# Performance work log

Hardware: AMD Instinct MI355X
Metric: run time of the kernel (lower is better)

## Reference

```python
import jax, jax.numpy as jnp
import numpy as np

DIM, E_DIM, HID = 512, 1024, 256
N_EXP, N_MIC, TOP_K, TOP_K_MIC = 8, 325, 2, 8
EPS_LN = 1e-5


def _layernorm(x, g, b):
    mu = x.mean(-1, keepdims=True)
    var = ((x - mu) ** 2).mean(-1, keepdims=True)
    return (x - mu) / jnp.sqrt(var + EPS_LN) * g + b


def setup_inputs() -> dict:
    key = jax.random.key(0)
    ks = jax.random.split(key, 20)
    s = 0.02
    return {
        "x": jax.random.normal(ks[0], (2, 512, DIM), jnp.float32),
        "router_w": jax.random.normal(ks[1], (N_EXP, DIM), jnp.float32) * s,
        "router_b": jnp.zeros((N_EXP,), jnp.float32),
        "exp_w1": jax.random.normal(ks[2], (N_EXP, E_DIM, DIM), jnp.float32) * s,
        "exp_b1": jnp.zeros((N_EXP, E_DIM), jnp.float32),
        "exp_w2": jax.random.normal(ks[3], (N_EXP, DIM, E_DIM), jnp.float32) * s,
        "exp_b2": jnp.zeros((N_EXP, DIM), jnp.float32),
        "mrouter_w": jax.random.normal(ks[4], (N_MIC, DIM), jnp.float32) * s,
        "mrouter_b": jnp.zeros((N_MIC,), jnp.float32),
        "mic_w1": jax.random.normal(ks[5], (N_MIC, HID, DIM), jnp.float32) * s,
        "mic_b1": jnp.zeros((N_MIC, HID), jnp.float32),
        "mic_w2": jax.random.normal(ks[6], (N_MIC, DIM, HID), jnp.float32) * s,
        "mic_b2": jnp.zeros((N_MIC, DIM), jnp.float32),
        "mic_g": jnp.ones((N_MIC, DIM), jnp.float32),
        "mic_beta": jnp.zeros((N_MIC, DIM), jnp.float32),
        "norm_g": jnp.ones((DIM,), jnp.float32),
        "norm_b": jnp.zeros((DIM,), jnp.float32),
    }


def _forward(x, router_w, router_b, exp_w1, exp_b1, exp_w2, exp_b2,
             mrouter_w, mrouter_b, mic_w1, mic_b1, mic_w2, mic_b2,
             mic_g, mic_beta, norm_g, norm_b):
    B, S, D = x.shape
    xf = x.reshape(-1, D)  # [T, D]

    # ---- expert routing (top-2 of 8) ----
    probs = jax.nn.softmax(xf @ router_w.T + router_b, axis=-1)
    topp, topi = jax.lax.top_k(probs, TOP_K)
    topp = topp / (topp.sum(-1, keepdims=True) + 1e-8)

    # dense compute over 8 experts, combine with top-k weights
    h = jax.nn.gelu(jnp.einsum('td,ehd->teh', xf, exp_w1) + exp_b1, approximate=False)
    ye = jnp.einsum('teh,edh->ted', h, exp_w2) + exp_b2  # [T, E, D]
    comb_w = (jax.nn.one_hot(topi, N_EXP, dtype=xf.dtype) * topp[..., None]).sum(1)  # [T, E]
    eo = jnp.einsum('te,ted->td', comb_w, ye)

    # ---- micro routing (top-8 of 325) ----
    mprobs = jax.nn.softmax(eo @ mrouter_w.T + mrouter_b, axis=-1)
    mtopp, mtopi = jax.lax.top_k(mprobs, TOP_K_MIC)
    mtopp = mtopp / (mtopp.sum(-1, keepdims=True) + 1e-8)

    def micro_slot(eo, p, idx):
        # gather per-token micro params, batched GEMV dispatch
        hm = jax.nn.gelu(jnp.einsum('td,thd->th', eo, mic_w1[idx]) + mic_b1[idx],
                         approximate=False)
        ym = jnp.einsum('th,tdh->td', hm, mic_w2[idx]) + mic_b2[idx]
        n = _layernorm(eo + ym, mic_g[idx], mic_beta[idx])
        return p[:, None] * n

    micro_slot = jax.checkpoint(micro_slot, static_argnums=())
    mo = jnp.zeros_like(eo)
    for k in range(TOP_K_MIC):  # small fixed loop over slots
        mo = mo + micro_slot(eo, mtopp[:, k], mtopi[:, k])

    combined = (eo + 0.1 * mo).reshape(B, S, D)
    return _layernorm(combined, norm_g, norm_b)


def reference(x, router_w, router_b, exp_w1, exp_b1, exp_w2, exp_b2,
              mrouter_w, mrouter_b, mic_w1, mic_b1, mic_w2, mic_b2,
              mic_g, mic_beta, norm_g, norm_b):
    return _forward(x, router_w, router_b, exp_w1, exp_b1, exp_w2, exp_b2,
                    mrouter_w, mrouter_b, mic_w1, mic_b1, mic_w2, mic_b2,
                    mic_g, mic_beta, norm_g, norm_b)
```

## Files before the change

kernel.cpp:

```cpp
#include <hip/hip_runtime.h>
#include <hip/hip_bf16.h>
#include <math.h>

#define T_TOK 1024
#define DIMM  512
#define EDIM  1024
#define HIDD  256
#define NEXP  8
#define NMIC  325
#define E16TILES 136
#define MTILES  840
#define NPAIR_M 8192

typedef __attribute__((ext_vector_type(8))) short bf16x8;
typedef __attribute__((ext_vector_type(4))) float f32x4;

__device__ __forceinline__ float dot4(float4 a, float4 b) {
    return a.x*b.x + a.y*b.y + a.z*b.z + a.w*b.w;
}
__device__ __forceinline__ float gelu_exact(float x) {
    return 0.5f * x * (1.0f + erff(x * 0.70710678118654752f));
}
__device__ __forceinline__ float wave_sum(float v) {
    #pragma unroll
    for (int o = 32; o; o >>= 1) v += __shfl_xor(v, o);
    return v;
}
__device__ __forceinline__ short f2bf(float f) {
    union { __hip_bfloat16 h; short s; } u;
    u.h = __float2bfloat16(f);
    return u.s;
}
__device__ __forceinline__ bf16x8 cvt8(float4 a, float4 b) {
    bf16x8 r;
    r[0]=f2bf(a.x); r[1]=f2bf(a.y); r[2]=f2bf(a.z); r[3]=f2bf(a.w);
    r[4]=f2bf(b.x); r[5]=f2bf(b.y); r[6]=f2bf(b.z); r[7]=f2bf(b.w);
    return r;
}

__global__ void k_router(const float* __restrict__ x, const float* __restrict__ rw,
                         const float* __restrict__ rb, int* __restrict__ eidx,
                         float* __restrict__ ew, int* __restrict__ ecnt) {
    int wave = threadIdx.x >> 6, lane = threadIdx.x & 63;
    int t = blockIdx.x * 4 + wave;
    if (t >= T_TOK) return;
    const float* xr = x + (size_t)t * DIMM;
    float xv[8];
    #pragma unroll
    for (int j = 0; j < 8; ++j) xv[j] = xr[lane + 64*j];
    float p[NEXP];
    #pragma unroll
    for (int e = 0; e < NEXP; ++e) {
        const float* wr = rw + (size_t)e * DIMM;
        float a = 0.f;
        #pragma unroll
        for (int j = 0; j < 8; ++j) a += xv[j] * wr[lane + 64*j];
        p[e] = wave_sum(a) + rb[e];
    }
    float m = p[0];
    #pragma unroll
    for (int e = 1; e < NEXP; ++e) m = fmaxf(m, p[e]);
    float Z = 0.f;
    #pragma unroll
    for (int e = 0; e < NEXP; ++e) { p[e] = expf(p[e] - m); Z += p[e]; }
    #pragma unroll
    for (int e = 0; e < NEXP; ++e) p[e] /= Z;
    int i1 = 0; float v1 = p[0];
    #pragma unroll
    for (int e = 1; e < NEXP; ++e) if (p[e] > v1) { v1 = p[e]; i1 = e; }
    int i2 = -1; float v2 = -1.f;
    #pragma unroll
    for (int e = 0; e < NEXP; ++e) if (e != i1 && p[e] > v2) { v2 = p[e]; i2 = e; }
    float s = v1 + v2 + 1e-8f;
    if (lane == 0) {
        eidx[t*2] = i1; eidx[t*2+1] = i2;
        ew[t*2] = v1 / s; ew[t*2+1] = v2 / s;
        atomicAdd(&ecnt[i1], 1); atomicAdd(&ecnt[i2], 1);
    }
}

__global__ void k_scan(const int* __restrict__ cnt, int n, int pm,
                       int* __restrict__ off, int* __restrict__ cur,
                       int2* __restrict__ tiles, int* __restrict__ ntile) {
    __shared__ int s[512], s2[512];
    int tid = threadIdx.x;
    int v  = (tid < n) ? cnt[tid] : 0;
    int tc = (v + pm - 1) / pm;
    s[tid] = v; s2[tid] = tc;
    __syncthreads();
    for (int d = 1; d < 512; d <<= 1) {
        int a = (tid >= d) ? s[tid-d] : 0;
        int b = (tid >= d) ? s2[tid-d] : 0;
        __syncthreads();
        s[tid] += a; s2[tid] += b;
        __syncthreads();
    }
    int myoff = s[tid] - v, tb = s2[tid] - tc;
    if (tid < n) { off[tid] = myoff; cur[tid] = myoff; }
    if (tid == n-1) off[n] = s[tid];
    if (tid == 511) *ntile = s2[511];
    for (int j = 0; j < tc; ++j) tiles[tb + j] = make_int2(tid, myoff + j*pm);
}

__global__ void k_scatter(const int* __restrict__ idx, const float* __restrict__ w,
                          int total, int S, int* __restrict__ cur,
                          int* __restrict__ ptok, float* __restrict__ pw,
                          int* __restrict__ pmi) {
    int g = blockIdx.x * blockDim.x + threadIdx.x;
    if (g >= total) return;
    int t = g / S;
    int e = idx[g];
    int pos = atomicAdd(&cur[e], 1);
    ptok[pos] = t; pw[pos] = w[g]; pmi[pos] = e;
}

__global__ __launch_bounds__(256) void k_effn1(
    const float* __restrict__ x, const float* __restrict__ w1, const float* __restrict__ b1,
    const int2* __restrict__ tiles, const int* __restrict__ ntile,
    const int* __restrict__ eoff, const int* __restrict__ ep_tok,
    float* __restrict__ hbuf) {
    if ((int)blockIdx.x >= *ntile) return;
    int2 tl = tiles[blockIdx.x];
    int e = tl.x, pbase = tl.y;
    int m = min(16, eoff[e+1] - pbase);
    __shared__ float4 xs[16][128];
    __shared__ int tok_s[16];
    int tid = threadIdx.x;
    if (tid < 16) tok_s[tid] = ep_tok[pbase + ((tid < m) ? tid : 0)];
    __syncthreads();
    const float4* x4 = (const float4*)x;
    for (int q = tid; q < 16*128; q += 256) {
        int i = q >> 7, k = q & 127;
        xs[i][k] = x4[(size_t)tok_s[i] * 128 + k];
    }
    __syncthreads();
    int c = blockIdx.y * 256 + tid;
    const float4* wr = (const float4*)(w1 + ((size_t)e * EDIM + c) * DIMM);
    float acc[16];
    #pragma unroll
    for (int i = 0; i < 16; ++i) acc[i] = 0.f;
    for (int kk = 0; kk < 128; ++kk) {
        float4 wv = wr[kk];
        #pragma unroll
        for (int i = 0; i < 16; ++i) acc[i] += dot4(wv, xs[i][kk]);
    }
    float bb = b1[(size_t)e * EDIM + c];
    for (int i = 0; i < m; ++i)
        hbuf[(size_t)(pbase + i) * EDIM + c] = gelu_exact(acc[i] + bb);
}

__global__ __launch_bounds__(256) void k_effn2(
    const float* __restrict__ hbuf, const float* __restrict__ w2, const float* __restrict__ b2,
    const int2* __restrict__ tiles, const int* __restrict__ ntile,
    const int* __restrict__ eoff, const int* __restrict__ ep_tok, const float* __restrict__ ep_w,
    float* __restrict__ eo) {
    if ((int)blockIdx.x >= *ntile) return;
    int2 tl = tiles[blockIdx.x];
    int e = tl.x, pbase = tl.y;
    int m = min(16, eoff[e+1] - pbase);
    int kc = blockIdx.z;
    __shared__ float4 hs[16][128];
    __shared__ int tok_s[16];
    __shared__ float pw_s[16];
    int tid = threadIdx.x;
    if (tid < 16) {
        int ok = tid < m;
        tok_s[tid] = ok ? ep_tok[pbase + tid] : 0;
        pw_s[tid]  = ok ? ep_w[pbase + tid] : 0.f;
    }
    __syncthreads();
    const float4* h4 = (const float4*)hbuf;
    for (int q = tid; q < 16*128; q += 256) {
        int i = q >> 7, k = q & 127;
        hs[i][k] = h4[(size_t)(pbase + ((i < m) ? i : 0)) * 256 + kc * 128 + k];
    }
    __syncthreads();
    int c = blockIdx.y * 256 + tid;
    const float4* wr = (const float4*)(w2 + ((size_t)e * DIMM + c) * EDIM + (size_t)kc * 512);
    float acc[16];
    #pragma unroll
    for (int i = 0; i < 16; ++i) acc[i] = 0.f;
    for (int kk = 0; kk < 128; ++kk) {
        float4 wv = wr[kk];
        #pragma unroll
        for (int i = 0; i < 16; ++i) acc[i] += dot4(wv, hs[i][kk]);
    }
    float bb = (kc == 0) ? b2[(size_t)e * DIMM + c] : 0.f;
    for (int i = 0; i < m; ++i) {
        float val = (acc[i] + bb) * pw_s[i];
        atomicAdd(&eo[(size_t)tok_s[i] * DIMM + c], val);
    }
}

__global__ __launch_bounds__(384) void k_mlog(
    const float* __restrict__ eo, const float* __restrict__ mw, const float* __restrict__ mb,
    float* __restrict__ mlog) {
    int t0 = blockIdx.x * 4;
    __shared__ float4 es[4][128];
    int tid = threadIdx.x;
    const float4* eo4 = (const float4*)eo;
    for (int q = tid; q < 4*128; q += 384) {
        int i = q >> 7, k = q & 127;
        es[i][k] = eo4[(size_t)(t0 + i) * 128 + k];
    }
    __syncthreads();
    if (tid < NMIC) {
        const float4* wr = (const float4*)(mw + (size_t)tid * DIMM);
        float acc[4] = {0.f, 0.f, 0.f, 0.f};
        for (int kk = 0; kk < 128; ++kk) {
            float4 wv = wr[kk];
            #pragma unroll
            for (int i = 0; i < 4; ++i) acc[i] += dot4(wv, es[i][kk]);
        }
        float bb = mb[tid];
        #pragma unroll
        for (int i = 0; i < 4; ++i) mlog[(size_t)(t0 + i) * NMIC + tid] = acc[i] + bb;
    }
}

__global__ void k_mtop(const float* __restrict__ mlog, int* __restrict__ mtopi,
                       float* __restrict__ mtopp, int* __restrict__ mcnt) {
    int wave = threadIdx.x >> 6, lane = threadIdx.x & 63;
    int t = blockIdx.x * 4 + wave;
    if (t >= T_TOK) return;
    float v[6]; int vi[6];
    #pragma unroll
    for (int j = 0; j < 6; ++j) {
        int n = lane + 64*j;
        vi[j] = n;
        v[j] = (n < NMIC) ? mlog[(size_t)t * NMIC + n] : -1e30f;
    }
    float M = v[0];
    #pragma unroll
    for (int j = 1; j < 6; ++j) M = fmaxf(M, v[j]);
    #pragma unroll
    for (int o = 32; o; o >>= 1) M = fmaxf(M, __shfl_xor(M, o));
    float Z = 0.f;
    #pragma unroll
    for (int j = 0; j < 6; ++j) Z += expf(v[j] - M);
    Z = wave_sum(Z);
    float bk[8]; int bi[8];
    for (int k = 0; k < 8; ++k) {
        float lv = v[0]; int li = vi[0];
        #pragma unroll
        for (int j = 1; j < 6; ++j)
            if (v[j] > lv) { lv = v[j]; li = vi[j]; }
        #pragma unroll
        for (int o = 32; o; o >>= 1) {
            float ov = __shfl_xor(lv, o); int oi = __shfl_xor(li, o);
            if (ov > lv || (ov == lv && oi < li)) { lv = ov; li = oi; }
        }
        bk[k] = expf(lv - M) / Z; bi[k] = li;
        #pragma unroll
        for (int j = 0; j < 6; ++j) if (vi[j] == li) v[j] = -1e30f;
    }
    float s = 0.f;
    #pragma unroll
    for (int k = 0; k < 8; ++k) s += bk[k];
    s += 1e-8f;
    if (lane == 0) {
        for (int k = 0; k < 8; ++k) {
            mtopi[t*8 + k] = bi[k];
            mtopp[t*8 + k] = bk[k] / s;
            atomicAdd(&mcnt[bi[k]], 1);
        }
    }
}

__global__ __launch_bounds__(256) void k_mffn1(
    const float* __restrict__ eo, const float* __restrict__ w1, const float* __restrict__ b1,
    const int2* __restrict__ tiles, const int* __restrict__ ntile,
    const int* __restrict__ moff, const int* __restrict__ mp_tok,
    short* __restrict__ ghbuf) {
    if ((int)blockIdx.x >= *ntile) return;
    int2 tl = tiles[blockIdx.x];
    int mi = tl.x, pbase = tl.y;
    int pm = min(16, moff[mi+1] - pbase);
    int by = blockIdx.y;
    __shared__ __align__(16) short eof[8192];
    __shared__ __align__(16) short hf[2048];
    __shared__ int tok_s[16];
    int tid = threadIdx.x;
    if (tid < 16) tok_s[tid] = mp_tok[pbase + ((tid < pm) ? tid : 0)];
    __syncthreads();
    int m0 = tid & 15;
    const float4* eorow = (const float4*)(eo + (size_t)tok_s[m0] * DIMM);
    for (int kk = tid >> 4; kk < 128; kk += 16) {
        float4 v = eorow[kk];
        int off = ((kk >> 3) * 512) + ((((kk >> 1) & 3) * 16 + m0) * 8) + ((kk & 1) * 4);
        short4 s4; s4.x = f2bf(v.x); s4.y = f2bf(v.y); s4.z = f2bf(v.z); s4.w = f2bf(v.w);
        *(short4*)(eof + off) = s4;
    }
    __syncthreads();
    int wave = tid >> 6, lane = tid & 63;
    int quad = lane >> 4, lcol = lane & 15;
    f32x4 zero = {0.f, 0.f, 0.f, 0.f};
    f32x4 accA[2];
    accA[0] = zero; accA[1] = zero;
    const float* w1base = w1 + (size_t)mi * HIDD * DIMM;
    for (int ks = 0; ks < 16; ++ks) {
        bf16x8 a = *(bf16x8*)(eof + ks*512 + lane*8);
        int kb = ks*32 + quad*8;
        #pragma unroll
        for (int q = 0; q < 2; ++q) {
            int n = by*128 + wave*32 + q*16 + lcol;
            const float* wp = w1base + (size_t)n * DIMM + kb;
            float4 wa = *(const float4*)wp;
            float4 wb = *(const float4*)(wp + 4);
            accA[q] = __builtin_amdgcn_mfma_f32_16x16x32_bf16(a, cvt8(wa, wb), accA[q], 0, 0, 0);
        }
    }
    #pragma unroll
    for (int q = 0; q < 2; ++q) {
        int hp = wave*32 + q*16 + lcol;
        float bb = b1[(size_t)mi * HIDD + by*128 + hp];
        int obase = ((hp >> 5) * 512) + (((hp >> 3) & 3) * 16) * 8 + (hp & 7);
        #pragma unroll
        for (int r = 0; r < 4; ++r) {
            int mm = quad*4 + r;
            hf[obase + mm*8] = f2bf(gelu_exact(accA[q][r] + bb));
        }
    }
    __syncthreads();
    short* gh = ghbuf + (size_t)blockIdx.x * 4096 + (size_t)by * 2048;
    ((int4*)gh)[tid] = ((const int4*)hf)[tid];
}

__global__ __launch_bounds__(256) void k_mffn2(
    const short* __restrict__ ghbuf, const float* __restrict__ w2, const float* __restrict__ b2,
    const int2* __restrict__ tiles, const int* __restrict__ ntile, const int* __restrict__ moff,
    float* __restrict__ ybuf) {
    if ((int)blockIdx.x >= *ntile) return;
    int2 tl = tiles[blockIdx.x];
    int mi = tl.x, pbase = tl.y;
    int pm = min(16, moff[mi+1] - pbase);
    int by = blockIdx.y;
    int tid = threadIdx.x, wave = tid >> 6, lane = tid & 63;
    int quad = lane >> 4, lcol = lane & 15;
    const short* gh = ghbuf + (size_t)blockIdx.x * 4096;
    f32x4 zero = {0.f, 0.f, 0.f, 0.f};
    f32x4 accB[4];
    #pragma unroll
    for (int q = 0; q < 4; ++q) accB[q] = zero;
    const float* w2base = w2 + (size_t)mi * DIMM * HIDD;
    for (int ks = 0; ks < 8; ++ks) {
        bf16x8 a = *(const bf16x8*)(gh + ks*512 + lane*8);
        int kb = ks*32 + quad*8;
        #pragma unroll
        for (int q = 0; q < 4; ++q) {
            int d = by*256 + wave*64 + q*16 + lcol;
            const float* wp = w2base + (size_t)d * HIDD + kb;
            float4 wa = *(const float4*)wp;
            float4 wb = *(const float4*)(wp + 4);
            accB[q] = __builtin_amdgcn_mfma_f32_16x16x32_bf16(a, cvt8(wa, wb), accB[q], 0, 0, 0);
        }
    }
    #pragma unroll
    for (int q = 0; q < 4; ++q) {
        int d = by*256 + wave*64 + q*16 + lcol;
        float bb = b2[(size_t)mi * DIMM + d];
        #pragma unroll
        for (int r = 0; r < 4; ++r) {
            int mm = quad*4 + r;
            if (mm < pm) ybuf[(size_t)(pbase + mm) * DIMM + d] = accB[q][r] + bb;
        }
    }
}

__global__ __launch_bounds__(256) void k_mln(
    const float* __restrict__ ybuf, const float* __restrict__ eo,
    const float* __restrict__ g, const float* __restrict__ beta,
    const int* __restrict__ mp_tok, const float* __restrict__ mp_w,
    const int* __restrict__ mp_mi, float* __restrict__ mo) {
    int wave = threadIdx.x >> 6, lane = threadIdx.x & 63;
    int p = blockIdx.x * 4 + wave;
    int t = mp_tok[p];
    int mi = mp_mi[p];
    float pw = mp_w[p];
    const float* yr = ybuf + (size_t)p * DIMM;
    const float* er = eo + (size_t)t * DIMM;
    float vv[8];
    float sum = 0.f;
    #pragma unroll
    for (int j = 0; j < 8; ++j) {
        int d = lane + 64*j;
        vv[j] = yr[d] + er[d];
        sum += vv[j];
    }
    sum = wave_sum(sum);
    float mu = sum * (1.f/512.f);
    float var = 0.f;
    #pragma unroll
    for (int j = 0; j < 8; ++j) { float d0 = vv[j] - mu; var += d0*d0; }
    var = wave_sum(var) * (1.f/512.f);
    float rstd = rsqrtf(var + 1e-5f);
    #pragma unroll
    for (int j = 0; j < 8; ++j) {
        int d = lane + 64*j;
        float nj = (vv[j] - mu) * rstd * g[(size_t)mi * DIMM + d] + beta[(size_t)mi * DIMM + d];
        atomicAdd(&mo[(size_t)t * DIMM + d], pw * nj);
    }
}

__global__ void k_final(const float* __restrict__ eo, const float* __restrict__ mo,
                        const float* __restrict__ g, const float* __restrict__ b,
                        float* __restrict__ out) {
    int wave = threadIdx.x >> 6, lane = threadIdx.x & 63;
    int t = blockIdx.x * 4 + wave;
    if (t >= T_TOK) return;
    float vv[8];
    float sum = 0.f;
    #pragma unroll
    for (int j = 0; j < 8; ++j) {
        int d = lane + 64*j;
        vv[j] = eo[(size_t)t * DIMM + d] + 0.1f * mo[(size_t)t * DIMM + d];
        sum += vv[j];
    }
    sum = wave_sum(sum);
    float mu = sum * (1.f/512.f);
    float var = 0.f;
    #pragma unroll
    for (int j = 0; j < 8; ++j) { float d0 = vv[j] - mu; var += d0*d0; }
    var = wave_sum(var) * (1.f/512.f);
    float rstd = rsqrtf(var + 1e-5f);
    #pragma unroll
    for (int j = 0; j < 8; ++j) {
        int d = lane + 64*j;
        out[(size_t)t * DIMM + d] = (vv[j] - mu) * rstd * g[d] + b[d];
    }
}

extern "C" void kernel_launch(void* const* d_in, const int* in_sizes, int n_in,
                              void* d_out, int out_size, void* d_ws, size_t ws_size,
                              hipStream_t stream) {
    const float* x    = (const float*)d_in[0];
    const float* rw   = (const float*)d_in[1];
    const float* rb   = (const float*)d_in[2];
    const float* ew1  = (const float*)d_in[3];
    const float* eb1  = (const float*)d_in[4];
    const float* ew2  = (const float*)d_in[5];
    const float* eb2  = (const float*)d_in[6];
    const float* mrw  = (const float*)d_in[7];
    const float* mrb  = (const float*)d_in[8];
    const float* mw1  = (const float*)d_in[9];
    const float* mb1  = (const float*)d_in[10];
    const float* mw2  = (const float*)d_in[11];
    const float* mb2  = (const float*)d_in[12];
    const float* mg   = (const float*)d_in[13];
    const float* mbeta= (const float*)d_in[14];
    const float* ng   = (const float*)d_in[15];
    const float* nb   = (const float*)d_in[16];
    float* out = (float*)d_out;

    char* w = (char*)d_ws;
    auto alloc = [&](size_t bytes) -> char* {
        char* p = w;
        w += (bytes + 255) & ~(size_t)255;
        return p;
    };
    float* eo    = (float*)alloc((size_t)T_TOK * DIMM * 4);
    float* mo    = (float*)alloc((size_t)T_TOK * DIMM * 4);
    float* hbuf  = (float*)alloc((size_t)2048 * EDIM * 4);
    float* ybuf  = (float*)alloc((size_t)NPAIR_M * DIMM * 4);
    float* mlog  = (float*)alloc((size_t)T_TOK * NMIC * 4);
    float* ewts  = (float*)alloc(2048 * 4);
    float* mtopp = (float*)alloc(8192 * 4);
    float* ep_w  = (float*)alloc(2048 * 4);
    float* mp_w  = (float*)alloc(8192 * 4);
    int*   eidx  = (int*)alloc(2048 * 4);
    int*   mtopi = (int*)alloc(8192 * 4);
    int*   cnts  = (int*)alloc((NEXP + NMIC) * 4);
    int*   ecnt  = cnts;
    int*   mcnt  = cnts + NEXP;
    int*   eoff  = (int*)alloc((NEXP + 1) * 4);
    int*   ecur  = (int*)alloc(NEXP * 4);
    int*   moff  = (int*)alloc((NMIC + 1) * 4);
    int*   mcur  = (int*)alloc(NMIC * 4);
    int2*  etile = (int2*)alloc(E16TILES * 8);
    int2*  mtile = (int2*)alloc(MTILES * 8);
    int*   entile= (int*)alloc(4);
    int*   mntile= (int*)alloc(4);
    int*   ep_tok= (int*)alloc(2048 * 4);
    int*   mp_tok= (int*)alloc(8192 * 4);
    int*   ep_mi = (int*)alloc(2048 * 4);
    int*   mp_mi = (int*)alloc(8192 * 4);
    short* ghbuf = (short*)hbuf;

    hipMemsetAsync(eo, 0, (size_t)2 * T_TOK * DIMM * 4, stream);
    hipMemsetAsync(cnts, 0, (NEXP + NMIC) * 4, stream);

    k_router <<<T_TOK/4, 256, 0, stream>>>(x, rw, rb, eidx, ewts, ecnt);
    k_scan   <<<1, 512, 0, stream>>>(ecnt, NEXP, 16, eoff, ecur, etile, entile);
    k_scatter<<<(T_TOK*2 + 255)/256, 256, 0, stream>>>(eidx, ewts, T_TOK*2, 2, ecur, ep_tok, ep_w, ep_mi);
    k_effn1  <<<dim3(E16TILES, 4, 1), 256, 0, stream>>>(x, ew1, eb1, etile, entile, eoff, ep_tok, hbuf);
    k_effn2  <<<dim3(E16TILES, 2, 2), 256, 0, stream>>>(hbuf, ew2, eb2, etile, entile, eoff, ep_tok, ep_w, eo);
    k_mlog   <<<T_TOK/4, 384, 0, stream>>>(eo, mrw, mrb, mlog);
    k_mtop   <<<T_TOK/4, 256, 0, stream>>>(mlog, mtopi, mtopp, mcnt);
    k_scan   <<<1, 512, 0, stream>>>(mcnt, NMIC, 16, moff, mcur, mtile, mntile);
    k_scatter<<<(T_TOK*8 + 255)/256, 256, 0, stream>>>(mtopi, mtopp, T_TOK*8, 8, mcur, mp_tok, mp_w, mp_mi);
    k_mffn1  <<<dim3(MTILES, 2, 1), 256, 0, stream>>>(eo, mw1, mb1, mtile, mntile, moff, mp_tok, ghbuf);
    k_mffn2  <<<dim3(MTILES, 2, 1), 256, 0, stream>>>(ghbuf, mw2, mb2, mtile, mntile, moff, ybuf);
    k_mln    <<<NPAIR_M/4, 256, 0, stream>>>(ybuf, eo, mg, mbeta, mp_tok, mp_w, mp_mi, mo);
    k_final  <<<T_TOK/4, 256, 0, stream>>>(eo, mo, ng, nb, out);
}
```

Baseline: 724.0 us.

## Run expert FFN GEMMs on fp16 MFMA with hi/lo split precision

The expert FFN kernels move from scalar fp32 FMA loops to fp16 MFMA. Weights and activations are split into hi and lo fp16 halves, with lo scaled by 4096, and three MFMAs per tile recover near-fp32 accuracy. The hidden activations are written as pre-laid-out MFMA fragments per tile, so the second FFN reads them directly without a shared-memory staging pass. This cuts the FMA-bound compute, at the cost of two extra per-call kernels that split the 16M weight elements, which adds memory traffic on every call.

Result: faster. 697.9 us (-3.6%).

```diff
diff --git a/kernel.cpp b/kernel.cpp
--- a/kernel.cpp
+++ b/kernel.cpp
@@ -13,6 +13,7 @@
 #define NPAIR_M 8192
 
 typedef __attribute__((ext_vector_type(8))) short bf16x8;
+typedef __attribute__((ext_vector_type(8))) _Float16 f16x8;
 typedef __attribute__((ext_vector_type(4))) float f32x4;
 
 __device__ __forceinline__ float dot4(float4 a, float4 b) {
@@ -31,11 +32,15 @@
     u.h = __float2bfloat16(f);
     return u.s;
 }
-__device__ __forceinline__ bf16x8 cvt8(float4 a, float4 b) {
-    bf16x8 r;
-    r[0]=f2bf(a.x); r[1]=f2bf(a.y); r[2]=f2bf(a.z); r[3]=f2bf(a.w);
-    r[4]=f2bf(b.x); r[5]=f2bf(b.y); r[6]=f2bf(b.z); r[7]=f2bf(b.w);
-    return r;
+__device__ __forceinline__ short f2h(float f) {
+    union { _Float16 h; short s; } u;
+    u.h = (_Float16)f;
+    return u.s;
+}
+__device__ __forceinline__ float h2f(short s) {
+    union { _Float16 h; short s; } u;
+    u.s = s;
+    return (float)u.h;
 }
 
 __global__ void k_router(const float* __restrict__ x, const float* __restrict__ rw,
@@ -114,43 +119,105 @@
     ptok[pos] = t; pw[pos] = w[g]; pmi[pos] = e;
 }
 
+__global__ __launch_bounds__(256) void k_wsplit(const float* __restrict__ w,
+                                                short* __restrict__ hi,
+                                                short* __restrict__ lo, int n4) {
+    int g = blockIdx.x * blockDim.x + threadIdx.x;
+    if (g >= n4) return;
+    float4 v = ((const float4*)w)[g];
+    short4 h4, l4;
+    h4.x = f2h(v.x); l4.x = f2h((v.x - h2f(h4.x)) * 4096.f);
+    h4.y = f2h(v.y); l4.y = f2h((v.y - h2f(h4.y)) * 4096.f);
+    h4.z = f2h(v.z); l4.z = f2h((v.z - h2f(h4.z)) * 4096.f);
+    h4.w = f2h(v.w); l4.w = f2h((v.w - h2f(h4.w)) * 4096.f);
+    ((short4*)hi)[g] = h4;
+    ((short4*)lo)[g] = l4;
+}
+
 __global__ __launch_bounds__(256) void k_effn1(
-    const float* __restrict__ x, const float* __restrict__ w1, const float* __restrict__ b1,
+    const float* __restrict__ x, const short* __restrict__ w1h, const short* __restrict__ w1l,
+    const float* __restrict__ b1,
     const int2* __restrict__ tiles, const int* __restrict__ ntile,
     const int* __restrict__ eoff, const int* __restrict__ ep_tok,
-    float* __restrict__ hbuf) {
+    short* __restrict__ ghhi, short* __restrict__ ghlo) {
     if ((int)blockIdx.x >= *ntile) return;
     int2 tl = tiles[blockIdx.x];
     int e = tl.x, pbase = tl.y;
     int m = min(16, eoff[e+1] - pbase);
-    __shared__ float4 xs[16][128];
+    int by = blockIdx.y;
+    __shared__ __align__(16) short xh[8192];
+    __shared__ __align__(16) short xl[8192];
     __shared__ int tok_s[16];
     int tid = threadIdx.x;
     if (tid < 16) tok_s[tid] = ep_tok[pbase + ((tid < m) ? tid : 0)];
     __syncthreads();
-    const float4* x4 = (const float4*)x;
-    for (int q = tid; q < 16*128; q += 256) {
-        int i = q >> 7, k = q & 127;
-        xs[i][k] = x4[(size_t)tok_s[i] * 128 + k];
-    }
-    __syncthreads();
-    int c = blockIdx.y * 256 + tid;
-    const float4* wr = (const float4*)(w1 + ((size_t)e * EDIM + c) * DIMM);
-    float acc[16];
-    #pragma unroll
-    for (int i = 0; i < 16; ++i) acc[i] = 0.f;
-    for (int kk = 0; kk < 128; ++kk) {
-        float4 wv = wr[kk];
-        #pragma unroll
-        for (int i = 0; i < 16; ++i) acc[i] += dot4(wv, xs[i][kk]);
-    }
-    float bb = b1[(size_t)e * EDIM + c];
-    for (int i = 0; i < m; ++i)
-        hbuf[(size_t)(pbase + i) * EDIM + c] = gelu_exact(acc[i] + bb);
+    int m0 = tid & 15;
+    const float4* xrow = (const float4*)(x + (size_t)tok_s[m0] * DIMM);
+    for (int kk = tid >> 4; kk < 128; kk += 16) {
+        float4 v = xrow[kk];
+        int off = ((kk >> 3) * 512) + ((((kk >> 1) & 3) * 16 + m0) * 8) + ((kk & 1) * 4);
+        short4 h4, l4;
+        h4.x = f2h(v.x); l4.x = f2h((v.x - h2f(h4.x)) * 4096.f);
+        h4.y = f2h(v.y); l4.y = f2h((v.y - h2f(h4.y)) * 4096.f);
+        h4.z = f2h(v.z); l4.z = f2h((v.z - h2f(h4.z)) * 4096.f);
+        h4.w = f2h(v.w); l4.w = f2h((v.w - h2f(h4.w)) * 4096.f);
+        *(short4*)(xh + off) = h4;
+        *(short4*)(xl + off) = l4;
+    }
+    __syncthreads();
+    int wave = tid >> 6, lane = tid & 63;
+    int quad = lane >> 4, lcol = lane & 15;
+    f32x4 zero = {0.f, 0.f, 0.f, 0.f};
+    f32x4 acc0[8], acc1[8];
+    #pragma unroll
+    for (int q = 0; q < 8; ++q) { acc0[q] = zero; acc1[q] = zero; }
+    const short* w1hb = w1h + (size_t)e * EDIM * DIMM;
+    const short* w1lb = w1l + (size_t)e * EDIM * DIMM;
+    for (int ks = 0; ks < 16; ++ks) {
+        f16x8 ah = *(const f16x8*)(xh + ks*512 + lane*8);
+        f16x8 al = *(const f16x8*)(xl + ks*512 + lane*8);
+        int kb = ks*32 + quad*8;
+        #pragma unroll
+        for (int q = 0; q < 8; ++q) {
+            int n = by*512 + wave*128 + q*16 + lcol;
+            size_t wo = (size_t)n * DIMM + kb;
+            f16x8 wh = *(const f16x8*)(w1hb + wo);
+            f16x8 wl = *(const f16x8*)(w1lb + wo);
+            acc0[q] = __builtin_amdgcn_mfma_f32_16x16x32_f16(ah, wh, acc0[q], 0, 0, 0);
+            acc1[q] = __builtin_amdgcn_mfma_f32_16x16x32_f16(al, wh, acc1[q], 0, 0, 0);
+            acc1[q] = __builtin_amdgcn_mfma_f32_16x16x32_f16(ah, wl, acc1[q], 0, 0, 0);
+        }
+    }
+    __syncthreads();
+    #pragma unroll
+    for (int q = 0; q < 8; ++q) {
+        int hp = wave*128 + q*16 + lcol;
+        float bb = b1[(size_t)e * EDIM + by*512 + hp];
+        int obase = ((hp >> 5) * 512) + (((hp >> 3) & 3) * 16) * 8 + (hp & 7);
+        #pragma unroll
+        for (int r = 0; r < 4; ++r) {
+            int mm = quad*4 + r;
+            float hv = gelu_exact(acc0[q][r] + acc1[q][r] * (1.f/4096.f) + bb);
+            short hh = f2h(hv);
+            xh[obase + mm*8] = hh;
+            xl[obase + mm*8] = f2h((hv - h2f(hh)) * 4096.f);
+        }
+    }
+    __syncthreads();
+    short* dh = ghhi + (size_t)blockIdx.x * 16384 + (size_t)by * 8192;
+    short* dl = ghlo + (size_t)blockIdx.x * 16384 + (size_t)by * 8192;
+    const int4* sh = (const int4*)xh;
+    const int4* sl = (const int4*)xl;
+    #pragma unroll
+    for (int j = 0; j < 4; ++j) {
+        ((int4*)dh)[tid + 256*j] = sh[tid + 256*j];
+        ((int4*)dl)[tid + 256*j] = sl[tid + 256*j];
+    }
 }
 
 __global__ __launch_bounds__(256) void k_effn2(
-    const float* __restrict__ hbuf, const float* __restrict__ w2, const float* __restrict__ b2,
+    const short* __restrict__ ghhi, const short* __restrict__ ghlo,
+    const short* __restrict__ w2h, const short* __restrict__ w2l, const float* __restrict__ b2,
     const int2* __restrict__ tiles, const int* __restrict__ ntile,
     const int* __restrict__ eoff, const int* __restrict__ ep_tok, const float* __restrict__ ep_w,
     float* __restrict__ eo) {
@@ -158,8 +225,7 @@
     int2 tl = tiles[blockIdx.x];
     int e = tl.x, pbase = tl.y;
     int m = min(16, eoff[e+1] - pbase);
-    int kc = blockIdx.z;
-    __shared__ float4 hs[16][128];
+    int by = blockIdx.y;
     __shared__ int tok_s[16];
     __shared__ float pw_s[16];
     int tid = threadIdx.x;
@@ -169,26 +235,43 @@
         pw_s[tid]  = ok ? ep_w[pbase + tid] : 0.f;
     }
     __syncthreads();
-    const float4* h4 = (const float4*)hbuf;
-    for (int q = tid; q < 16*128; q += 256) {
-        int i = q >> 7, k = q & 127;
-        hs[i][k] = h4[(size_t)(pbase + ((i < m) ? i : 0)) * 256 + kc * 128 + k];
-    }
-    __syncthreads();
-    int c = blockIdx.y * 256 + tid;
-    const float4* wr = (const float4*)(w2 + ((size_t)e * DIMM + c) * EDIM + (size_t)kc * 512);
-    float acc[16];
-    #pragma unroll
-    for (int i = 0; i < 16; ++i) acc[i] = 0.f;
-    for (int kk = 0; kk < 128; ++kk) {
-        float4 wv = wr[kk];
-        #pragma unroll
-        for (int i = 0; i < 16; ++i) acc[i] += dot4(wv, hs[i][kk]);
-    }
-    float bb = (kc == 0) ? b2[(size_t)e * DIMM + c] : 0.f;
-    for (int i = 0; i < m; ++i) {
-        float val = (acc[i] + bb) * pw_s[i];
-        atomicAdd(&eo[(size_t)tok_s[i] * DIMM + c], val);
+    int wave = tid >> 6, lane = tid & 63;
+    int quad = lane >> 4, lcol = lane & 15;
+    const short* ahb = ghhi + (size_t)blockIdx.x * 16384;
+    const short* alb = ghlo + (size_t)blockIdx.x * 16384;
+    f32x4 zero = {0.f, 0.f, 0.f, 0.f};
+    f32x4 acc0[4], acc1[4];
+    #pragma unroll
+    for (int q = 0; q < 4; ++q) { acc0[q] = zero; acc1[q] = zero; }
+    const short* w2hb = w2h + (size_t)e * DIMM * EDIM;
+    const short* w2lb = w2l + (size_t)e * DIMM * EDIM;
+    for (int ks = 0; ks < 32; ++ks) {
+        f16x8 ah = *(const f16x8*)(ahb + ks*512 + lane*8);
+        f16x8 al = *(const f16x8*)(alb + ks*512 + lane*8);
+        int kb = ks*32 + quad*8;
+        #pragma unroll
+        for (int q = 0; q < 4; ++q) {
+            int d = by*256 + wave*64 + q*16 + lcol;
+            size_t wo = (size_t)d * EDIM + kb;
+            f16x8 wh = *(const f16x8*)(w2hb + wo);
+            f16x8 wl = *(const f16x8*)(w2lb + wo);
+            acc0[q] = __builtin_amdgcn_mfma_f32_16x16x32_f16(ah, wh, acc0[q], 0, 0, 0);
+            acc1[q] = __builtin_amdgcn_mfma_f32_16x16x32_f16(al, wh, acc1[q], 0, 0, 0);
+            acc1[q] = __builtin_amdgcn_mfma_f32_16x16x32_f16(ah, wl, acc1[q], 0, 0, 0);
+        }
+    }
+    #pragma unroll
+    for (int q = 0; q < 4; ++q) {
+        int d = by*256 + wave*64 + q*16 + lcol;
+        float bb = b2[(size_t)e * DIMM + d];
+        #pragma unroll
+        for (int r = 0; r < 4; ++r) {
+            int mm = quad*4 + r;
+            if (mm < m) {
+                float val = (acc0[q][r] + acc1[q][r] * (1.f/4096.f) + bb) * pw_s[mm];
+                atomicAdd(&eo[(size_t)tok_s[mm] * DIMM + d], val);
+            }
+        }
     }
 }
 
@@ -307,7 +390,10 @@
             const float* wp = w1base + (size_t)n * DIMM + kb;
             float4 wa = *(const float4*)wp;
             float4 wb = *(const float4*)(wp + 4);
-            accA[q] = __builtin_amdgcn_mfma_f32_16x16x32_bf16(a, cvt8(wa, wb), accA[q], 0, 0, 0);
+            bf16x8 bfr;
+            bfr[0]=f2bf(wa.x); bfr[1]=f2bf(wa.y); bfr[2]=f2bf(wa.z); bfr[3]=f2bf(wa.w);
+            bfr[4]=f2bf(wb.x); bfr[5]=f2bf(wb.y); bfr[6]=f2bf(wb.z); bfr[7]=f2bf(wb.w);
+            accA[q] = __builtin_amdgcn_mfma_f32_16x16x32_bf16(a, bfr, accA[q], 0, 0, 0);
         }
     }
     #pragma unroll
@@ -352,7 +438,10 @@
             const float* wp = w2base + (size_t)d * HIDD + kb;
             float4 wa = *(const float4*)wp;
             float4 wb = *(const float4*)(wp + 4);
-            accB[q] = __builtin_amdgcn_mfma_f32_16x16x32_bf16(a, cvt8(wa, wb), accB[q], 0, 0, 0);
+            bf16x8 bfr;
+            bfr[0]=f2bf(wa.x); bfr[1]=f2bf(wa.y); bfr[2]=f2bf(wa.z); bfr[3]=f2bf(wa.w);
+            bfr[4]=f2bf(wb.x); bfr[5]=f2bf(wb.y); bfr[6]=f2bf(wb.z); bfr[7]=f2bf(wb.w);
+            accB[q] = __builtin_amdgcn_mfma_f32_16x16x32_bf16(a, bfr, accB[q], 0, 0, 0);
         }
     }
     #pragma unroll
@@ -458,10 +547,19 @@
         w += (bytes + 255) & ~(size_t)255;
         return p;
     };
+    const size_t WELEM = (size_t)NEXP * EDIM * DIMM;
     float* eo    = (float*)alloc((size_t)T_TOK * DIMM * 4);
     float* mo    = (float*)alloc((size_t)T_TOK * DIMM * 4);
-    float* hbuf  = (float*)alloc((size_t)2048 * EDIM * 4);
-    float* ybuf  = (float*)alloc((size_t)NPAIR_M * DIMM * 4);
+    short* wspl  = (short*)alloc(WELEM * 2 * 4);
+    short* w1h   = wspl;
+    short* w1l   = wspl + WELEM;
+    short* w2h   = wspl + 2*WELEM;
+    short* w2l   = wspl + 3*WELEM;
+    float* ybuf  = (float*)wspl;
+    short* gfrag = (short*)alloc((size_t)E16TILES * 16384 * 2 * 2);
+    short* ehhi  = gfrag;
+    short* ehlo  = gfrag + (size_t)E16TILES * 16384;
+    short* ghbuf = gfrag;
     float* mlog  = (float*)alloc((size_t)T_TOK * NMIC * 4);
     float* ewts  = (float*)alloc(2048 * 4);
     float* mtopp = (float*)alloc(8192 * 4);
@@ -484,16 +582,18 @@
     int*   mp_tok= (int*)alloc(8192 * 4);
     int*   ep_mi = (int*)alloc(2048 * 4);
     int*   mp_mi = (int*)alloc(8192 * 4);
-    short* ghbuf = (short*)hbuf;
 
     hipMemsetAsync(eo, 0, (size_t)2 * T_TOK * DIMM * 4, stream);
     hipMemsetAsync(cnts, 0, (NEXP + NMIC) * 4, stream);
 
+    int n4 = (int)(WELEM / 4);
+    k_wsplit <<<n4/256, 256, 0, stream>>>(ew1, w1h, w1l, n4);
+    k_wsplit <<<n4/256, 256, 0, stream>>>(ew2, w2h, w2l, n4);
     k_router <<<T_TOK/4, 256, 0, stream>>>(x, rw, rb, eidx, ewts, ecnt);
     k_scan   <<<1, 512, 0, stream>>>(ecnt, NEXP, 16, eoff, ecur, etile, entile);
     k_scatter<<<(T_TOK*2 + 255)/256, 256, 0, stream>>>(eidx, ewts, T_TOK*2, 2, ecur, ep_tok, ep_w, ep_mi);
-    k_effn1  <<<dim3(E16TILES, 4, 1), 256, 0, stream>>>(x, ew1, eb1, etile, entile, eoff, ep_tok, hbuf);
-    k_effn2  <<<dim3(E16TILES, 2, 2), 256, 0, stream>>>(hbuf, ew2, eb2, etile, entile, eoff, ep_tok, ep_w, eo);
+    k_effn1  <<<dim3(E16TILES, 2, 1), 256, 0, stream>>>(x, w1h, w1l, eb1, etile, entile, eoff, ep_tok, ehhi, ehlo);
+    k_effn2  <<<dim3(E16TILES, 2, 1), 256, 0, stream>>>(ehhi, ehlo, w2h, w2l, eb2, etile, entile, eoff, ep_tok, ep_w, eo);
     k_mlog   <<<T_TOK/4, 384, 0, stream>>>(eo, mrw, mrb, mlog);
     k_mtop   <<<T_TOK/4, 256, 0, stream>>>(mlog, mtopi, mtopp, mcnt);
     k_scan   <<<1, 512, 0, stream>>>(mcnt, NMIC, 16, moff, mcur, mtile, mntile);
```
